# Kernel optimization log

Hardware: AMD Instinct MI355X
Metric: run time of the kernel (lower is better)

Reference implementation:

```python
import jax, jax.numpy as jnp
import numpy as np

ITER_STEPS = 2  # matches init_kwargs iteration_steps


def setup_inputs() -> dict:
    key = jax.random.key(0)
    ks = jax.random.split(key, 7)
    B, N, D = 16, 1024, 128
    s = 1.0 / np.sqrt(D).astype(np.float32)
    return {
        "node": jax.random.normal(ks[0], (B, N, D), jnp.float32),
        "node_mask": jax.random.randint(ks[1], (B, N), 0, 2, jnp.int32),
        "graph": jax.random.randint(ks[2], (B, N, N), 0, 2, jnp.int32),
        "w_weight": jax.random.normal(ks[3], (D, 1), jnp.float32) * s,
        "b_weight": jnp.zeros((1,), jnp.float32),
        "w_self": jax.random.normal(ks[4], (D, D), jnp.float32) * s,
        "b_self": jnp.zeros((D,), jnp.float32),
        "w_left": jax.random.normal(ks[5], (D, D), jnp.float32) * s,
        "w_right": jax.random.normal(ks[6], (D, D), jnp.float32) * s,
    }


def reference(node, node_mask, graph, w_weight, b_weight, w_self, b_self, w_left, w_right):
    B, N, D = node.shape
    dt = node.dtype
    nm = node_mask.astype(dt)
    g = graph.astype(dt)  # graph[:, :N, :N] slice is identity here
    diag = jnp.eye(N, dtype=dt)
    # pairwise validity mask, zero diagonal (no self loops)
    pair = nm[:, None, :] * nm[:, :, None] * (1.0 - diag)
    gl = pair * g            # edges present in graph
    gr = pair * (1.0 - g)    # complement edges
    nnum = gl.sum(-1) + gr.sum(-1)
    # replace_masked_values(nnum, nnum>=1, 1): avoid div-by-zero for isolated nodes
    nnum = jnp.where(nnum >= 1.0, nnum, jnp.ones((), dt))
    ws = []
    for _ in range(ITER_STEPS):
        node_weight = jax.nn.sigmoid(node @ w_weight + b_weight)[..., 0]  # [B, N]
        ws.append(node_weight)
        self_info = node @ w_self + b_self
        # replace_masked_values(weight_bcast, mask, 0) == weight * mask (mask is 0/1)
        left = jnp.einsum('bij,bjd->bid', node_weight[:, None, :] * gl, node @ w_left)
        right = jnp.einsum('bij,bjd->bid', node_weight[:, None, :] * gr, node @ w_right)
        node = jax.nn.relu(self_info + (left + right) / nnum[..., None])
    all_node_weight = jnp.stack(ws, axis=1)  # [B, ITER_STEPS, N]
    return node, all_node_weight
```

## Files before the change

kernel.cpp:

```cpp
#include <hip/hip_runtime.h>
#include <math.h>


constexpr int B = 16, N = 1024, D = 128, ITERS = 2;

typedef unsigned short u16;
typedef unsigned char u8;
typedef unsigned int u32;
typedef __attribute__((ext_vector_type(8))) short short8v;
typedef __attribute__((ext_vector_type(4))) unsigned int uint4v;
typedef __attribute__((ext_vector_type(4))) float float4v;

__device__ inline u16 f32_to_bf16(float f) {
  u32 bits = __float_as_uint(f);
  bits += 0x7FFFu + ((bits >> 16) & 1u);
  return (u16)(bits >> 16);
}

__device__ __forceinline__ void map_brt(int blk, int& b, int& rt) {
  int slot = blk >> 3;
  b = ((slot >> 6) << 3) | (blk & 7);
  rt = slot & 63;
}

__global__ __launch_bounds__(256) void wpack_kernel(
    const float* __restrict__ w_self, const float* __restrict__ w_left,
    const float* __restrict__ w_right, const int* __restrict__ mask,
    u16* __restrict__ wsF, u16* __restrict__ wlF, u16* __restrict__ wrF,
    float* __restrict__ sb) {
  int blk = blockIdx.x, tid = threadIdx.x;
  if (blk < 12) {
    int widx = blk >> 2, seg = blk & 3;
    const float* W = (widx == 0) ? w_self : (widx == 1) ? w_left : w_right;
    u16* WF = (widx == 0) ? wsF : (widx == 1) ? wlF : wrF;
#pragma unroll
    for (int q = 0; q < 16; ++q) {
      int o = seg * 4096 + q * 256 + tid;
      int e = o & 7, lane = (o >> 3) & 63, ks = (o >> 9) & 3, cblk = o >> 11;
      int c = cblk * 16 + (lane & 15);
      int k = ks * 32 + ((lane >> 4) & 3) * 8 + e;
      WF[o] = f32_to_bf16(W[k * 128 + c]);
    }
  } else {
    int b = tid >> 4, seg = tid & 15;
    const int* mp = mask + b * N + seg * 64;
    int s = 0;
    for (int q = 0; q < 64; ++q) s += mp[q];
    float fs = (float)s;
    fs += __shfl_xor(fs, 8, 16);
    fs += __shfl_xor(fs, 4, 16);
    fs += __shfl_xor(fs, 2, 16);
    fs += __shfl_xor(fs, 1, 16);
    if (seg == 0) sb[b] = fs;
  }
}

__device__ __forceinline__ void prep_body(
    float (*nlds)[132], float* wmrow, float* invrow, int b, int rt, int tid,
    const int* __restrict__ mask, const float* __restrict__ w_weight,
    const float* __restrict__ b_weight, const float* __restrict__ b_self,
    const u16* __restrict__ wsF, const u16* __restrict__ wlF,
    const u16* __restrict__ wrF, const float* __restrict__ sb,
    float* __restrict__ outw_t, float* __restrict__ nsadj, u16* __restrict__ xF,
    float* __restrict__ part) {
  int r0 = rt * 16;
  if (tid < 128) {
    int r = tid >> 3, jj = tid & 7;
    float acc = 0.f;
#pragma unroll
    for (int q = 0; q < 4; ++q) {
      float4 wv = *(const float4*)(w_weight + jj * 16 + q * 4);
      const float* np = &nlds[r][jj * 16 + q * 4];
      acc += np[0] * wv.x + np[1] * wv.y + np[2] * wv.z + np[3] * wv.w;
    }
    acc += __shfl_xor(acc, 4, 8);
    acc += __shfl_xor(acc, 2, 8);
    acc += __shfl_xor(acc, 1, 8);
    if (jj == 0) {
      float w = 1.f / (1.f + expf(-(acc + b_weight[0])));
      outw_t[b * (ITERS * N) + r0 + r] = w;
      float nm = (float)mask[b * N + r0 + r];
      float nnum = fmaxf(nm * (sb[b] - nm), 1.f);
      wmrow[r] = w * nm;
      invrow[r] = nm / nnum;
    }
  }
  __syncthreads();

  int w = tid >> 6, lane = tid & 63;
  int l15 = lane & 15, lg = lane >> 4;
  int ch = w * 32;

  short8v af[4];
#pragma unroll
  for (int ks = 0; ks < 4; ++ks) {
    float tmp[8];
    *(float4*)&tmp[0] = *(const float4*)&nlds[l15][ks * 32 + lg * 8];
    *(float4*)&tmp[4] = *(const float4*)&nlds[l15][ks * 32 + lg * 8 + 4];
    short8v t;
#pragma unroll
    for (int e = 0; e < 8; ++e) t[e] = (short)f32_to_bf16(tmp[e]);
    af[ks] = t;
  }

  float4v aNR[2], aNL[2], aNS[2];
#define RUN_GEMM(WF, ACC)                                                          \
  {                                                                                \
    _Pragma("unroll") for (int cf = 0; cf < 2; ++cf) {                             \
      ACC[cf] = (float4v){0.f, 0.f, 0.f, 0.f};                                     \
      int cblk = w * 2 + cf;                                                       \
      const u16* bp = (WF) + (((cblk * 4) * 64 + lane) << 3);                      \
      _Pragma("unroll") for (int ks = 0; ks < 4; ++ks) {                           \
        short8v bf = *(const short8v*)(bp + ks * 512);                             \
        ACC[cf] =                                                                  \
            __builtin_amdgcn_mfma_f32_16x16x32_bf16(af[ks], bf, ACC[cf], 0, 0, 0); \
      }                                                                            \
    }                                                                              \
  }
  RUN_GEMM(wrF, aNR);
  RUN_GEMM(wlF, aNL);
  RUN_GEMM(wsF, aNS);
#undef RUN_GEMM

  float wmv[4], invv[4];
#pragma unroll
  for (int j = 0; j < 4; ++j) {
    int rloc = lg * 4 + j;
    wmv[j] = wmrow[rloc];
    invv[j] = invrow[rloc];
  }
  int kch = rt >> 1;
  int lane_f = ((rt & 1) * 2 + (lg >> 1)) * 16;
  int e0 = (lg & 1) * 4;
  float pv[2] = {0.f, 0.f};
#pragma unroll
  for (int cf = 0; cf < 2; ++cf) {
    int col = ch + cf * 16 + l15;
    float bsv = b_self[col];
    u16 xb[4];
#pragma unroll
    for (int j = 0; j < 4; ++j) {
      float x = wmv[j] * (aNL[cf][j] - aNR[cf][j]);
      float v = wmv[j] * aNR[cf][j];
      pv[cf] += v;
      nsadj[((size_t)b * N + r0 + lg * 4 + j) * D + col] =
          aNS[cf][j] + bsv - invv[j] * v;
      xb[j] = f32_to_bf16(x);
    }
    int cblk = w * 2 + cf;
    size_t fi = ((((size_t)b * 8 + cblk) * 32 + kch) * 64 + lane_f + l15) * 8 + e0;
    *(ushort4*)&xF[fi] = *(ushort4*)&xb[0];
  }
#pragma unroll
  for (int cf = 0; cf < 2; ++cf) {
    pv[cf] += __shfl_xor(pv[cf], 16);
    pv[cf] += __shfl_xor(pv[cf], 32);
  }
  if (lg == 0) {
#pragma unroll
    for (int cf = 0; cf < 2; ++cf)
      part[((size_t)b * 64 + rt) * 128 + ch + cf * 16 + l15] = pv[cf];
  }
}

__device__ __forceinline__ void agg_tile(
    const u8* __restrict__ gpk, const u16* __restrict__ xF,
    const float* __restrict__ part, const float* __restrict__ sb,
    const int* __restrict__ mask, const float* __restrict__ nsadj, int b, int r0,
    int tid, float (*accbuf)[16][132], float* vt_s, float ov[8]) {
  if (tid < 128) {
    float s = 0.f;
#pragma unroll
    for (int p = 0; p < 64; ++p) s += part[((size_t)b * 64 + p) * 128 + tid];
    vt_s[tid] = s;
  }
  int w = tid >> 6, lane = tid & 63;
  int l15 = lane & 15, lg = lane >> 4;
  int ks = w;
  const u8* gr = gpk + ((size_t)b * N + r0 + l15) * 128 + lg * 32 + ks * 8;
  uint2 q = *(const uint2*)gr;
  u32 qa[2] = {q.x, q.y};

  const u16* xb = xF + ((((size_t)b * 8) * 32 + ks * 8) * 64 + lane) * 8;

  float4v acc[8] = {{0.f, 0.f, 0.f, 0.f}, {0.f, 0.f, 0.f, 0.f},
                    {0.f, 0.f, 0.f, 0.f}, {0.f, 0.f, 0.f, 0.f},
                    {0.f, 0.f, 0.f, 0.f}, {0.f, 0.f, 0.f, 0.f},
                    {0.f, 0.f, 0.f, 0.f}, {0.f, 0.f, 0.f, 0.f}};
  short8v bcur[8], bnxt[8];
#pragma unroll
  for (int cf = 0; cf < 8; ++cf)
    bcur[cf] = *(const short8v*)(xb + cf * 16384);
#pragma unroll
  for (int cl = 0; cl < 8; ++cl) {
    if (cl + 1 < 8) {
#pragma unroll
      for (int cf = 0; cf < 8; ++cf)
        bnxt[cf] = *(const short8v*)(xb + cf * 16384 + (cl + 1) * 512);
    }
    u32 by = (qa[cl >> 2] >> ((cl & 3) * 8)) & 255u;
    u32 e0 = ((by & 1u) ? 0x3F80u : 0u) | ((by & 2u) ? 0x3F800000u : 0u);
    u32 e1 = ((by & 4u) ? 0x3F80u : 0u) | ((by & 8u) ? 0x3F800000u : 0u);
    u32 e2 = ((by & 16u) ? 0x3F80u : 0u) | ((by & 32u) ? 0x3F800000u : 0u);
    u32 e3 = ((by & 64u) ? 0x3F80u : 0u) | ((by & 128u) ? 0x3F800000u : 0u);
    uint4v ev = {e0, e1, e2, e3};
    short8v a = __builtin_bit_cast(short8v, ev);
#pragma unroll
    for (int cf = 0; cf < 8; ++cf)
      acc[cf] = __builtin_amdgcn_mfma_f32_16x16x32_bf16(a, bcur[cf], acc[cf], 0, 0, 0);
#pragma unroll
    for (int cf = 0; cf < 8; ++cf) bcur[cf] = bnxt[cf];
  }
#pragma unroll
  for (int cf = 0; cf < 8; ++cf)
#pragma unroll
    for (int j = 0; j < 4; ++j) accbuf[w][lg * 4 + j][cf * 16 + l15] = acc[cf][j];
  __syncthreads();

  int row = w * 4 + (lane >> 4);
  int colb = (tid & 15) * 8;
  int orow = r0 + row;
  float nm = (float)mask[b * N + orow];
  float sbv = sb[b];
  float nnum = fmaxf(nm * (sbv - nm), 1.f);
  float inv = nm / nnum;
  const float* nsp = nsadj + ((size_t)b * N + orow) * D + colb;
  float4 n0 = *(const float4*)nsp;
  float4 n1 = *(const float4*)(nsp + 4);
  float nsa[8] = {n0.x, n0.y, n0.z, n0.w, n1.x, n1.y, n1.z, n1.w};
#pragma unroll
  for (int e = 0; e < 8; ++e) {
    int c = colb + e;
    float m = accbuf[0][row][c] + accbuf[1][row][c] + accbuf[2][row][c] +
              accbuf[3][row][c] + vt_s[c];
    ov[e] = fmaxf(nsa[e] + inv * m, 0.f);
  }
}

__global__ __launch_bounds__(256, 4) void prep_pack_kernel(
    const float* __restrict__ node, const int* __restrict__ graph,
    const int* __restrict__ mask, const float* __restrict__ w_weight,
    const float* __restrict__ b_weight, const float* __restrict__ b_self,
    const u16* __restrict__ wsF, const u16* __restrict__ wlF,
    const u16* __restrict__ wrF, const float* __restrict__ sb,
    u8* __restrict__ gpk, float* __restrict__ outw, float* __restrict__ nsadjA,
    u16* __restrict__ xFA, float* __restrict__ partA) {
  __shared__ float nlds[16][132];
  __shared__ float wmrow[16], invrow[16];
  __shared__ u32 lbw[2][32];
  int tid = threadIdx.x;
  int b, rt;
  map_brt(blockIdx.x, b, rt);
  int r0 = rt * 16;

  {
    int rl = tid >> 7, j = tid & 127;
#pragma unroll
    for (int pp = 0; pp < 8; ++pp) {
      int i = r0 + pp * 2 + rl;
      const int* gp = graph + ((size_t)b * N + i) * N + j * 8;
      int4 a = *(const int4*)gp;
      int4 c = *(const int4*)(gp + 4);
      u32 by = (u32)(a.x != 0) | ((u32)(a.y != 0) << 1) | ((u32)(a.z != 0) << 2) |
               ((u32)(a.w != 0) << 3) | ((u32)(c.x != 0) << 4) |
               ((u32)(c.y != 0) << 5) | ((u32)(c.z != 0) << 6) |
               ((u32)(c.w != 0) << 7);
      if (j == (i >> 3)) by &= ~(1u << (i & 7));
      ((u8*)&lbw[rl][0])[(j & 3) * 32 + (j >> 2)] = (u8)by;
      __syncthreads();
      if (tid < 64) {
        int rl2 = tid >> 5, d = tid & 31;
        ((u32*)gpk)[((size_t)b * N + r0 + pp * 2 + rl2) * 32 + d] = lbw[rl2][d];
      }
      __syncthreads();
    }
  }

  const float* nbase = node + ((size_t)b * N + r0) * D;
#pragma unroll
  for (int p = 0; p < 2; ++p) {
    int g = p * 256 + tid;
    int row = g >> 5, c4 = g & 31;
    *(float4*)&nlds[row][c4 * 4] = *(const float4*)(nbase + row * 128 + c4 * 4);
  }
  __syncthreads();

  prep_body(nlds, wmrow, invrow, b, rt, tid, mask, w_weight, b_weight, b_self, wsF,
            wlF, wrF, sb, outw, nsadjA, xFA, partA);
}

__global__ __launch_bounds__(256, 3) void agg_prep_kernel(
    const u8* __restrict__ gpk, const int* __restrict__ mask,
    const float* __restrict__ w_weight, const float* __restrict__ b_weight,
    const float* __restrict__ b_self, const u16* __restrict__ wsF,
    const u16* __restrict__ wlF, const u16* __restrict__ wrF,
    const float* __restrict__ sb, const float* __restrict__ nsadjA,
    const u16* __restrict__ xFA, const float* __restrict__ partA,
    float* __restrict__ outw, float* __restrict__ nsadjB, u16* __restrict__ xFB,
    float* __restrict__ partB) {
  __shared__ float accbuf[4][16][132];
  __shared__ float vt_s[128];
  __shared__ float nlds[16][132];
  __shared__ float wmrow[16], invrow[16];
  int tid = threadIdx.x;
  int b, rt;
  map_brt(blockIdx.x, b, rt);
  int r0 = rt * 16;

  float ov[8];
  agg_tile(gpk, xFA, partA, sb, mask, nsadjA, b, r0, tid, accbuf, vt_s, ov);

  int row = (tid >> 6) * 4 + ((tid & 63) >> 4);
  int colb = (tid & 15) * 8;
#pragma unroll
  for (int e = 0; e < 8; ++e) nlds[row][colb + e] = ov[e];
  __syncthreads();

  prep_body(nlds, wmrow, invrow, b, rt, tid, mask, w_weight, b_weight, b_self, wsF,
            wlF, wrF, sb, outw + N , nsadjB, xFB, partB);
}

__global__ __launch_bounds__(256, 4) void agg_fin_kernel(
    const u8* __restrict__ gpk, const int* __restrict__ mask,
    const float* __restrict__ sb, const float* __restrict__ nsadjB,
    const u16* __restrict__ xFB, const float* __restrict__ partB,
    float* __restrict__ out) {
  __shared__ float accbuf[4][16][132];
  __shared__ float vt_s[128];
  int tid = threadIdx.x;
  int b, rt;
  map_brt(blockIdx.x, b, rt);
  int r0 = rt * 16;

  float ov[8];
  agg_tile(gpk, xFB, partB, sb, mask, nsadjB, b, r0, tid, accbuf, vt_s, ov);

  int row = (tid >> 6) * 4 + ((tid & 63) >> 4);
  int colb = (tid & 15) * 8;
  float* op = out + ((size_t)b * N + r0 + row) * D + colb;
  float4 o0 = {ov[0], ov[1], ov[2], ov[3]};
  float4 o1 = {ov[4], ov[5], ov[6], ov[7]};
  *(float4*)op = o0;
  *(float4*)(op + 4) = o1;
}

extern "C" void kernel_launch(void* const* d_in, const int* in_sizes, int n_in,
                              void* d_out, int out_size, void* d_ws, size_t ws_size,
                              hipStream_t stream) {
  const float* node0 = (const float*)d_in[0];
  const int* mask = (const int*)d_in[1];
  const int* graph = (const int*)d_in[2];
  const float* w_weight = (const float*)d_in[3];
  const float* b_weight = (const float*)d_in[4];
  const float* w_self = (const float*)d_in[5];
  const float* b_self = (const float*)d_in[6];
  const float* w_left = (const float*)d_in[7];
  const float* w_right = (const float*)d_in[8];
  float* out = (float*)d_out;
  float* outw = out + (size_t)B * N * D;

  char* ws = (char*)d_ws;
  const size_t MB = 1024 * 1024;
  float* nsadjA = (float*)ws;
  float* nsadjB = (float*)(ws + 8 * MB);
  u16* xFA = (u16*)(ws + 16 * MB);
  u16* xFB = (u16*)(ws + 20 * MB);
  u8* gpk = (u8*)(ws + 24 * MB);
  u16* wsF = (u16*)(ws + 26 * MB);
  u16* wlF = wsF + 16384;
  u16* wrF = wlF + 16384;
  float* partA = (float*)(ws + 26 * MB + 3 * 32768);
  float* partB = partA + (size_t)B * 64 * 128;
  float* sb = partB + (size_t)B * 64 * 128;

  wpack_kernel<<<13, 256, 0, stream>>>(w_self, w_left, w_right, mask, wsF, wlF,
                                       wrF, sb);
  prep_pack_kernel<<<1024, 256, 0, stream>>>(node0, graph, mask, w_weight,
                                             b_weight, b_self, wsF, wlF, wrF, sb,
                                             gpk, outw, nsadjA, xFA, partA);
  agg_prep_kernel<<<1024, 256, 0, stream>>>(gpk, mask, w_weight, b_weight, b_self,
                                            wsF, wlF, wrF, sb, nsadjA, xFA, partA,
                                            outw, nsadjB, xFB, partB);
  agg_fin_kernel<<<1024, 256, 0, stream>>>(gpk, mask, sb, nsadjB, xFB, partB, out);
}
```

Before: 66.05 us.

## Fold weight-pack kernel into prep kernel with atomic spin barrier

Removes the separate weight-pack/mask-sum launch by running it in the first 13 blocks of the prep kernel. The other blocks do their graph packing and node loads first, then spin on a global atomic counter before using the packed weights. The aggregation kernels also reuse one shared buffer for the node tile instead of a separate array, cutting LDS so agg_prep can use launch bounds of 4 blocks. The cost is an added memset launch and a spin-wait that only works because blocks 0-12 are dispatched first, with a timeout that could silently yield wrong data.

```diff
diff --git a/kernel.cpp b/kernel.cpp
--- a/kernel.cpp
+++ b/kernel.cpp
@@ -23,35 +23,11 @@
   rt = slot & 63;
 }
 
-__global__ __launch_bounds__(256) void wpack_kernel(
-    const float* __restrict__ w_self, const float* __restrict__ w_left,
-    const float* __restrict__ w_right, const int* __restrict__ mask,
-    u16* __restrict__ wsF, u16* __restrict__ wlF, u16* __restrict__ wrF,
-    float* __restrict__ sb) {
-  int blk = blockIdx.x, tid = threadIdx.x;
-  if (blk < 12) {
-    int widx = blk >> 2, seg = blk & 3;
-    const float* W = (widx == 0) ? w_self : (widx == 1) ? w_left : w_right;
-    u16* WF = (widx == 0) ? wsF : (widx == 1) ? wlF : wrF;
-#pragma unroll
-    for (int q = 0; q < 16; ++q) {
-      int o = seg * 4096 + q * 256 + tid;
-      int e = o & 7, lane = (o >> 3) & 63, ks = (o >> 9) & 3, cblk = o >> 11;
-      int c = cblk * 16 + (lane & 15);
-      int k = ks * 32 + ((lane >> 4) & 3) * 8 + e;
-      WF[o] = f32_to_bf16(W[k * 128 + c]);
-    }
-  } else {
-    int b = tid >> 4, seg = tid & 15;
-    const int* mp = mask + b * N + seg * 64;
-    int s = 0;
-    for (int q = 0; q < 64; ++q) s += mp[q];
-    float fs = (float)s;
-    fs += __shfl_xor(fs, 8, 16);
-    fs += __shfl_xor(fs, 4, 16);
-    fs += __shfl_xor(fs, 2, 16);
-    fs += __shfl_xor(fs, 1, 16);
-    if (seg == 0) sb[b] = fs;
+__device__ __forceinline__ void spin_ge(u32* p, u32 v) {
+  int t = 0;
+  while (__hip_atomic_load(p, __ATOMIC_ACQUIRE, __HIP_MEMORY_SCOPE_AGENT) < v) {
+    __builtin_amdgcn_s_sleep(1);
+    if (++t > (1 << 22)) break;
   }
 }
 
@@ -163,11 +139,11 @@
   }
 }
 
-__device__ __forceinline__ void agg_tile(
+__device__ __forceinline__ void agg_core(
     const u8* __restrict__ gpk, const u16* __restrict__ xF,
     const float* __restrict__ part, const float* __restrict__ sb,
     const int* __restrict__ mask, const float* __restrict__ nsadj, int b, int r0,
-    int tid, float (*accbuf)[16][132], float* vt_s, float ov[8]) {
+    int tid, float (*smA)[16][132], float (*smB)[132], float* vt_s, float ov[8]) {
   if (tid < 128) {
     float s = 0.f;
 #pragma unroll
@@ -189,8 +165,7 @@
                     {0.f, 0.f, 0.f, 0.f}, {0.f, 0.f, 0.f, 0.f}};
   short8v bcur[8], bnxt[8];
 #pragma unroll
-  for (int cf = 0; cf < 8; ++cf)
-    bcur[cf] = *(const short8v*)(xb + cf * 16384);
+  for (int cf = 0; cf < 8; ++cf) bcur[cf] = *(const short8v*)(xb + cf * 16384);
 #pragma unroll
   for (int cl = 0; cl < 8; ++cl) {
     if (cl + 1 < 8) {
@@ -207,14 +182,22 @@
     short8v a = __builtin_bit_cast(short8v, ev);
 #pragma unroll
     for (int cf = 0; cf < 8; ++cf)
-      acc[cf] = __builtin_amdgcn_mfma_f32_16x16x32_bf16(a, bcur[cf], acc[cf], 0, 0, 0);
+      acc[cf] =
+          __builtin_amdgcn_mfma_f32_16x16x32_bf16(a, bcur[cf], acc[cf], 0, 0, 0);
 #pragma unroll
     for (int cf = 0; cf < 8; ++cf) bcur[cf] = bnxt[cf];
   }
-#pragma unroll
-  for (int cf = 0; cf < 8; ++cf)
-#pragma unroll
-    for (int j = 0; j < 4; ++j) accbuf[w][lg * 4 + j][cf * 16 + l15] = acc[cf][j];
+  if (w < 3) {
+#pragma unroll
+    for (int cf = 0; cf < 8; ++cf)
+#pragma unroll
+      for (int j = 0; j < 4; ++j) smA[w][lg * 4 + j][cf * 16 + l15] = acc[cf][j];
+  } else {
+#pragma unroll
+    for (int cf = 0; cf < 8; ++cf)
+#pragma unroll
+      for (int j = 0; j < 4; ++j) smB[lg * 4 + j][cf * 16 + l15] = acc[cf][j];
+  }
   __syncthreads();
 
   int row = w * 4 + (lane >> 4);
@@ -231,8 +214,8 @@
 #pragma unroll
   for (int e = 0; e < 8; ++e) {
     int c = colb + e;
-    float m = accbuf[0][row][c] + accbuf[1][row][c] + accbuf[2][row][c] +
-              accbuf[3][row][c] + vt_s[c];
+    float m = smA[0][row][c] + smA[1][row][c] + smA[2][row][c] + smB[row][c] +
+              vt_s[c];
     ov[e] = fmaxf(nsa[e] + inv * m, 0.f);
   }
 }
@@ -241,16 +224,52 @@
     const float* __restrict__ node, const int* __restrict__ graph,
     const int* __restrict__ mask, const float* __restrict__ w_weight,
     const float* __restrict__ b_weight, const float* __restrict__ b_self,
-    const u16* __restrict__ wsF, const u16* __restrict__ wlF,
-    const u16* __restrict__ wrF, const float* __restrict__ sb,
+    const float* __restrict__ w_self, const float* __restrict__ w_left,
+    const float* __restrict__ w_right, u16* __restrict__ wsF,
+    u16* __restrict__ wlF, u16* __restrict__ wrF, float* __restrict__ sb,
     u8* __restrict__ gpk, float* __restrict__ outw, float* __restrict__ nsadjA,
-    u16* __restrict__ xFA, float* __restrict__ partA) {
+    u16* __restrict__ xFA, float* __restrict__ partA, u32* bar) {
+  int blk = blockIdx.x, tid = threadIdx.x;
+  if (blk < 13) {
+    if (blk < 12) {
+      int widx = blk >> 2, seg = blk & 3;
+      const float* W = (widx == 0) ? w_self : (widx == 1) ? w_left : w_right;
+      u16* WF = (widx == 0) ? wsF : (widx == 1) ? wlF : wrF;
+#pragma unroll
+      for (int q = 0; q < 16; ++q) {
+        int o = seg * 4096 + q * 256 + tid;
+        int e = o & 7, lane = (o >> 3) & 63, ks = (o >> 9) & 3, cblk = o >> 11;
+        int c = cblk * 16 + (lane & 15);
+        int k = ks * 32 + ((lane >> 4) & 3) * 8 + e;
+        WF[o] = f32_to_bf16(W[k * 128 + c]);
+      }
+    } else {
+      int b = tid >> 4, seg = tid & 15;
+      const int* mp = mask + b * N + seg * 64;
+      int s = 0;
+      for (int q = 0; q < 64; ++q) s += mp[q];
+      float fs = (float)s;
+      fs += __shfl_xor(fs, 8, 16);
+      fs += __shfl_xor(fs, 4, 16);
+      fs += __shfl_xor(fs, 2, 16);
+      fs += __shfl_xor(fs, 1, 16);
+      if (seg == 0) sb[b] = fs;
+    }
+    __threadfence();
+    __syncthreads();
+    if (tid == 0)
+      __hip_atomic_fetch_add(&bar[0], 1u, __ATOMIC_ACQ_REL,
+                             __HIP_MEMORY_SCOPE_AGENT);
+    return;
+  }
+
   __shared__ float nlds[16][132];
   __shared__ float wmrow[16], invrow[16];
   __shared__ u32 lbw[2][32];
-  int tid = threadIdx.x;
-  int b, rt;
-  map_brt(blockIdx.x, b, rt);
+  int pblk = blk - 13;
+  int slot = pblk >> 3;
+  int b = ((slot >> 6) << 3) | (pblk & 7);
+  int rt = slot & 63;
   int r0 = rt * 16;
 
   {
@@ -283,13 +302,14 @@
     int row = g >> 5, c4 = g & 31;
     *(float4*)&nlds[row][c4 * 4] = *(const float4*)(nbase + row * 128 + c4 * 4);
   }
+  if (tid == 0) spin_ge(&bar[0], 13);
   __syncthreads();
 
   prep_body(nlds, wmrow, invrow, b, rt, tid, mask, w_weight, b_weight, b_self, wsF,
             wlF, wrF, sb, outw, nsadjA, xFA, partA);
 }
 
-__global__ __launch_bounds__(256, 3) void agg_prep_kernel(
+__global__ __launch_bounds__(256, 4) void agg_prep_kernel(
     const u8* __restrict__ gpk, const int* __restrict__ mask,
     const float* __restrict__ w_weight, const float* __restrict__ b_weight,
     const float* __restrict__ b_self, const u16* __restrict__ wsF,
@@ -298,9 +318,9 @@
     const u16* __restrict__ xFA, const float* __restrict__ partA,
     float* __restrict__ outw, float* __restrict__ nsadjB, u16* __restrict__ xFB,
     float* __restrict__ partB) {
-  __shared__ float accbuf[4][16][132];
+  __shared__ float smA[3][16][132];
+  __shared__ float smB[16][132];
   __shared__ float vt_s[128];
-  __shared__ float nlds[16][132];
   __shared__ float wmrow[16], invrow[16];
   int tid = threadIdx.x;
   int b, rt;
@@ -308,15 +328,16 @@
   int r0 = rt * 16;
 
   float ov[8];
-  agg_tile(gpk, xFA, partA, sb, mask, nsadjA, b, r0, tid, accbuf, vt_s, ov);
+  agg_core(gpk, xFA, partA, sb, mask, nsadjA, b, r0, tid, smA, smB, vt_s, ov);
+  __syncthreads();
 
   int row = (tid >> 6) * 4 + ((tid & 63) >> 4);
   int colb = (tid & 15) * 8;
 #pragma unroll
-  for (int e = 0; e < 8; ++e) nlds[row][colb + e] = ov[e];
+  for (int e = 0; e < 8; ++e) smB[row][colb + e] = ov[e];
   __syncthreads();
 
-  prep_body(nlds, wmrow, invrow, b, rt, tid, mask, w_weight, b_weight, b_self, wsF,
+  prep_body(smB, wmrow, invrow, b, rt, tid, mask, w_weight, b_weight, b_self, wsF,
             wlF, wrF, sb, outw + N , nsadjB, xFB, partB);
 }
 
@@ -325,7 +346,8 @@
     const float* __restrict__ sb, const float* __restrict__ nsadjB,
     const u16* __restrict__ xFB, const float* __restrict__ partB,
     float* __restrict__ out) {
-  __shared__ float accbuf[4][16][132];
+  __shared__ float smA[3][16][132];
+  __shared__ float smB[16][132];
   __shared__ float vt_s[128];
   int tid = threadIdx.x;
   int b, rt;
@@ -333,7 +355,7 @@
   int r0 = rt * 16;
 
   float ov[8];
-  agg_tile(gpk, xFB, partB, sb, mask, nsadjB, b, r0, tid, accbuf, vt_s, ov);
+  agg_core(gpk, xFB, partB, sb, mask, nsadjB, b, r0, tid, smA, smB, vt_s, ov);
 
   int row = (tid >> 6) * 4 + ((tid & 63) >> 4);
   int colb = (tid & 15) * 8;
@@ -372,12 +394,13 @@
   float* partA = (float*)(ws + 26 * MB + 3 * 32768);
   float* partB = partA + (size_t)B * 64 * 128;
   float* sb = partB + (size_t)B * 64 * 128;
-
-  wpack_kernel<<<13, 256, 0, stream>>>(w_self, w_left, w_right, mask, wsF, wlF,
-                                       wrF, sb);
-  prep_pack_kernel<<<1024, 256, 0, stream>>>(node0, graph, mask, w_weight,
-                                             b_weight, b_self, wsF, wlF, wrF, sb,
-                                             gpk, outw, nsadjA, xFA, partA);
+  u32* bar = (u32*)(ws + 28 * MB);
+
+  hipMemsetAsync(bar, 0, 64, stream);
+  prep_pack_kernel<<<1037, 256, 0, stream>>>(node0, graph, mask, w_weight,
+                                             b_weight, b_self, w_self, w_left,
+                                             w_right, wsF, wlF, wrF, sb, gpk,
+                                             outw, nsadjA, xFA, partA, bar);
   agg_prep_kernel<<<1024, 256, 0, stream>>>(gpk, mask, w_weight, b_weight, b_self,
                                             wsF, wlF, wrF, sb, nsadjA, xFA, partA,
                                             outw, nsadjB, xFB, partB);
```

Result: slower. 78.21 us (+18.4%).

## Split graph bit-packing into dedicated blocks separate from prep work

Applied to the files above, without the earlier changes.

Graph bit-packing moves out of the per-row-tile prep blocks into 2048 dedicated blocks that each pack a contiguous slice of the graph with no shared-memory staging or barriers. The remaining 1024 blocks do only the node preprocessing. The goal is to spread the dominant 64MB graph read across more blocks and remove the per-row __syncthreads. The byte-wise global stores are uncoalesced scatter writes, and the prep blocks no longer overlap their own graph reads.

```diff
diff --git a/kernel.cpp b/kernel.cpp
--- a/kernel.cpp
+++ b/kernel.cpp
@@ -189,8 +189,7 @@
                     {0.f, 0.f, 0.f, 0.f}, {0.f, 0.f, 0.f, 0.f}};
   short8v bcur[8], bnxt[8];
 #pragma unroll
-  for (int cf = 0; cf < 8; ++cf)
-    bcur[cf] = *(const short8v*)(xb + cf * 16384);
+  for (int cf = 0; cf < 8; ++cf) bcur[cf] = *(const short8v*)(xb + cf * 16384);
 #pragma unroll
   for (int cl = 0; cl < 8; ++cl) {
     if (cl + 1 < 8) {
@@ -207,7 +206,8 @@
     short8v a = __builtin_bit_cast(short8v, ev);
 #pragma unroll
     for (int cf = 0; cf < 8; ++cf)
-      acc[cf] = __builtin_amdgcn_mfma_f32_16x16x32_bf16(a, bcur[cf], acc[cf], 0, 0, 0);
+      acc[cf] =
+          __builtin_amdgcn_mfma_f32_16x16x32_bf16(a, bcur[cf], acc[cf], 0, 0, 0);
 #pragma unroll
     for (int cf = 0; cf < 8; ++cf) bcur[cf] = bnxt[cf];
   }
@@ -237,7 +237,7 @@
   }
 }
 
-__global__ __launch_bounds__(256, 4) void prep_pack_kernel(
+__global__ __launch_bounds__(256, 4) void pack_prep_kernel(
     const float* __restrict__ node, const int* __restrict__ graph,
     const int* __restrict__ mask, const float* __restrict__ w_weight,
     const float* __restrict__ b_weight, const float* __restrict__ b_self,
@@ -247,18 +247,17 @@
     u16* __restrict__ xFA, float* __restrict__ partA) {
   __shared__ float nlds[16][132];
   __shared__ float wmrow[16], invrow[16];
-  __shared__ u32 lbw[2][32];
   int tid = threadIdx.x;
-  int b, rt;
-  map_brt(blockIdx.x, b, rt);
-  int r0 = rt * 16;
-
-  {
-    int rl = tid >> 7, j = tid & 127;
-#pragma unroll
-    for (int pp = 0; pp < 8; ++pp) {
-      int i = r0 + pp * 2 + rl;
-      const int* gp = graph + ((size_t)b * N + i) * N + j * 8;
+  int blk = blockIdx.x;
+
+  if (blk < 2048) {
+    int gidx = blk * 256 + tid;
+#pragma unroll
+    for (int it = 0; it < 4; ++it, gidx += 2048 * 256) {
+      int j = gidx & 127;
+      int rowg = gidx >> 7;
+      int i = rowg & (N - 1);
+      const int* gp = graph + ((size_t)rowg << 10) + j * 8;
       int4 a = *(const int4*)gp;
       int4 c = *(const int4*)(gp + 4);
       u32 by = (u32)(a.x != 0) | ((u32)(a.y != 0) << 1) | ((u32)(a.z != 0) << 2) |
@@ -266,15 +265,15 @@
                ((u32)(c.y != 0) << 5) | ((u32)(c.z != 0) << 6) |
                ((u32)(c.w != 0) << 7);
       if (j == (i >> 3)) by &= ~(1u << (i & 7));
-      ((u8*)&lbw[rl][0])[(j & 3) * 32 + (j >> 2)] = (u8)by;
-      __syncthreads();
-      if (tid < 64) {
-        int rl2 = tid >> 5, d = tid & 31;
-        ((u32*)gpk)[((size_t)b * N + r0 + pp * 2 + rl2) * 32 + d] = lbw[rl2][d];
-      }
-      __syncthreads();
-    }
-  }
+      gpk[((size_t)rowg << 7) + (j & 3) * 32 + (j >> 2)] = (u8)by;
+    }
+    return;
+  }
+
+  int pblk = blk - 2048;
+  int b, rt;
+  map_brt(pblk, b, rt);
+  int r0 = rt * 16;
 
   const float* nbase = node + ((size_t)b * N + r0) * D;
 #pragma unroll
@@ -375,7 +374,7 @@
 
   wpack_kernel<<<13, 256, 0, stream>>>(w_self, w_left, w_right, mask, wsF, wlF,
                                        wrF, sb);
-  prep_pack_kernel<<<1024, 256, 0, stream>>>(node0, graph, mask, w_weight,
+  pack_prep_kernel<<<3072, 256, 0, stream>>>(node0, graph, mask, w_weight,
                                              b_weight, b_self, wsF, wlF, wrF, sb,
                                              gpk, outw, nsadjA, xFA, partA);
   agg_prep_kernel<<<1024, 256, 0, stream>>>(gpk, mask, w_weight, b_weight, b_self,
```

Result: slower. 67.44 us (+2.1%).
